# Kernel optimization log

Measured on AMD Instinct MI355X. Metric: run time of the kernel, lower is better.

The kernel has to match this reference:

```python
import jax, jax.numpy as jnp
import numpy as np

B, T = 128, 2048
E, OUT, HID = 8, 32, 64          # num_experts, kan_out_features, gru_hidden_dim
GRID_SIZE, ORDER = 5, 3          # standard efficient-kan defaults
KCOEF = GRID_SIZE + ORDER        # B-spline basis functions per input feature


def make_grid():
    # extended knot grid on [-1, 1], length GRID_SIZE + 2*ORDER + 1
    h = 2.0 / GRID_SIZE
    return jnp.arange(-ORDER, GRID_SIZE + ORDER + 1, dtype=jnp.float32) * h - 1.0


def b_splines(x, grid):
    # x: [..., in_features] -> [..., in_features, KCOEF] via Cox-de Boor recursion
    x = x[..., None]
    b = ((x >= grid[:-1]) & (x < grid[1:])).astype(x.dtype)
    for k in range(1, ORDER + 1):
        left = (x - grid[:-(k + 1)]) / (grid[k:-1] - grid[:-(k + 1)])
        right = (grid[k + 1:] - x) / (grid[k + 1:] - grid[1:-k])
        b = left * b[..., :-1] + right * b[..., 1:]
    return b


def kan_moe(x, gate_w, gate_b, base_w, spline_w, grid):
    # x: [B,T,in=1]; dense softmax-gated mixture of KANLinear experts
    gate = jax.nn.softmax(x @ gate_w + gate_b, axis=-1)                 # [B,T,E]
    base_out = jnp.einsum('bti,eoi->bteo', jax.nn.silu(x), base_w)      # [B,T,E,OUT]
    bs = b_splines(x, grid).reshape(x.shape[0], x.shape[1], -1)         # [B,T,in*KCOEF]
    spline_out = jnp.einsum('btk,eok->bteo', bs, spline_w)              # [B,T,E,OUT]
    return jnp.einsum('bte,bteo->bto', gate, base_out + spline_out)     # [B,T,OUT]


def gru(x, w_ih, w_hh, b_ih, b_hh):
    # PyTorch GRU convention: gates ordered (r, z, n); batch_first semantics
    xp = jnp.einsum('btf,gf->btg', x, w_ih) + b_ih                      # [B,T,3H]

    def step(h, xt):
        hp = h @ w_hh.T + b_hh
        xr, xz, xn = jnp.split(xt, 3, axis=-1)
        hr, hz, hn = jnp.split(hp, 3, axis=-1)
        r = jax.nn.sigmoid(xr + hr)
        z = jax.nn.sigmoid(xz + hz)
        n = jnp.tanh(xn + r * hn)
        h = (1.0 - z) * n + z * h
        return h, h

    h0 = jnp.zeros((x.shape[0], HID), x.dtype)
    _, hs = jax.lax.scan(step, h0, jnp.swapaxes(xp, 0, 1))
    return jnp.swapaxes(hs, 0, 1)                                       # [B,T,H]


def setup_inputs() -> dict:
    key = jax.random.key(0)
    ks = jax.random.split(key, 12)
    def n(k, shape, scale=0.1):
        return jax.random.normal(k, shape, jnp.float32) * scale
    return {
        'a': jax.random.normal(ks[0], (B, T, 1), jnp.float32),
        'd': jax.random.normal(ks[1], (B, T, 1), jnp.float32),
        'gate_w_a': n(ks[2], (1, E)), 'gate_b_a': jnp.zeros((E,), jnp.float32),
        'base_w_a': n(ks[3], (E, OUT, 1)), 'spline_w_a': n(ks[4], (E, OUT, KCOEF)),
        'gate_w_d': n(ks[5], (1, E)), 'gate_b_d': jnp.zeros((E,), jnp.float32),
        'base_w_d': n(ks[6], (E, OUT, 1)), 'spline_w_d': n(ks[7], (E, OUT, KCOEF)),
        'conv_w': n(ks[8], (OUT, OUT, 5)), 'conv_b': jnp.zeros((OUT,), jnp.float32),
        'w_ih': n(ks[9], (3 * HID, OUT)), 'w_hh': n(ks[10], (3 * HID, HID)),
        'b_ih': jnp.zeros((3 * HID,), jnp.float32), 'b_hh': jnp.zeros((3 * HID,), jnp.float32),
    }


def reference(a, d, gate_w_a, gate_b_a, base_w_a, spline_w_a,
              gate_w_d, gate_b_d, base_w_d, spline_w_d,
              conv_w, conv_b, w_ih, w_hh, b_ih, b_hh):
    grid = make_grid()
    fa = kan_moe(a, gate_w_a, gate_b_a, base_w_a, spline_w_a, grid)     # trend features
    fd = kan_moe(d, gate_w_d, gate_b_d, base_w_d, spline_w_d, grid)     # residual features
    # TemporalBlock: permute -> Conv1d(padding='same') -> ReLU -> permute back
    xc = jnp.swapaxes(fa, 1, 2)                                         # [B,C,T]
    yc = jax.lax.conv_general_dilated(
        xc, conv_w, (1,), 'SAME', dimension_numbers=('NCH', 'OIH', 'NCH')
    ) + conv_b[None, :, None]
    trend = jnp.swapaxes(jax.nn.relu(yc), 1, 2)                         # [B,T,OUT]
    ctx = gru(fd, w_ih, w_hh, b_ih, b_hh)                               # [B,T,HID]
    # dropout is identity in eval mode
    return jnp.concatenate([trend, ctx], axis=-1)                       # [B,T,OUT+HID]
```

## Files before the change

### kernel.cpp

```cpp
#include <hip/hip_runtime.h>
#include <cstdint>

typedef _Float16 half2_t __attribute__((ext_vector_type(2)));

#define B_   128
#define T_   2048
#define E_   8
#define OUT_ 32
#define HID_ 64
#define KC_  8
#define TILE_A 128
#define NSEG 2
#define SPLIT 1088
#define WUPC 4
#define CH_  32
#define NCHB 34

__device__ __forceinline__ float frcp(float x) { return __builtin_amdgcn_rcpf(x); }
__device__ __forceinline__ float exp2_(float x) {
#if __has_builtin(__builtin_amdgcn_exp2f)
  return __builtin_amdgcn_exp2f(x);
#else
  return exp2f(x);
#endif
}
__device__ __forceinline__ float fsig(float x) { return frcp(1.0f + __expf(-x)); }

__device__ __forceinline__ float fdot2_(half2_t a, half2_t b, float c) {
#if __has_builtin(__builtin_amdgcn_fdot2)
  return __builtin_amdgcn_fdot2(a, b, c, false);
#else
  return fmaf((float)a.x, (float)b.x, fmaf((float)a.y, (float)b.y, c));
#endif
}

__device__ __forceinline__ half2_t u2h2(unsigned u) {
  return __builtin_bit_cast(half2_t, u);
}
__device__ __forceinline__ half2_t packh2(float a, float b) {
  half2_t h; h.x = (_Float16)a; h.y = (_Float16)b; return h;
}
__device__ __forceinline__ float rlanef(float v, int i) {
  return __int_as_float(__builtin_amdgcn_readlane(__float_as_int(v), i));
}
__device__ __forceinline__ unsigned rlaneu(unsigned v, int i) {
  return (unsigned)__builtin_amdgcn_readlane((int)v, i);
}

#define NLOG2E  (-1.4426950408889634f)
#define N2LOG2E (-2.8853900817779268f)

__device__ __forceinline__ void kan_scalars(float x, const float* gwr, const float* gbr,
                                            float& silu, float* gate, float* bs) {
  silu = x * fsig(x);
  float le[E_];
  float m = -1e30f;
#pragma unroll
  for (int e = 0; e < E_; ++e) { le[e] = fmaf(x, gwr[e], gbr[e]); m = fmaxf(m, le[e]); }
  float s = 0.f;
#pragma unroll
  for (int e = 0; e < E_; ++e) { gate[e] = __expf(le[e] - m); s += gate[e]; }
  float inv = frcp(s);
#pragma unroll
  for (int e = 0; e < E_; ++e) gate[e] *= inv;
  float g[12];
#pragma unroll
  for (int i = 0; i < 12; ++i) g[i] = (float)(i - 3) * 0.4f - 1.0f;
  float bb[11];
#pragma unroll
  for (int i = 0; i < 11; ++i) bb[i] = (x >= g[i] && x < g[i + 1]) ? 1.0f : 0.0f;
#pragma unroll
  for (int k = 1; k <= 3; ++k) {
#pragma unroll
    for (int i = 0; i < 11 - k; ++i) {
      const float dl = 1.0f / (g[i + k] - g[i]);
      const float dr = 1.0f / (g[i + k + 1] - g[i + 1]);
      float left  = (x - g[i]) * dl;
      float right = (g[i + k + 1] - x) * dr;
      bb[i] = left * bb[i] + right * bb[i + 1];
    }
  }
#pragma unroll
  for (int i = 0; i < KC_; ++i) bs[i] = bb[i];
}

__global__ __launch_bounds__(256, 1) void fused4_kernel(
    const float* __restrict__ a, const float* __restrict__ d,
    const float* __restrict__ gwa, const float* __restrict__ gba,
    const float* __restrict__ bwa, const float* __restrict__ swa,
    const float* __restrict__ gwd, const float* __restrict__ gbd,
    const float* __restrict__ bwd, const float* __restrict__ swd,
    const float* __restrict__ cw, const float* __restrict__ cb,
    const float* __restrict__ wih_g, const float* __restrict__ whh_g,
    const float* __restrict__ bih_g, const float* __restrict__ bhh_g,
    float* __restrict__ out)
{
  __shared__ __align__(16) char smem_[47360];
  const int tid = threadIdx.x;

  auto xqc = (uint2 (*)[CH_][64])smem_;
  auto hbc = (unsigned short*)(smem_ + 32768);

  const int bid = (int)blockIdx.x;
  const int b = bid & (B_ - 1);
  const int seg = bid >> 7;
  const int tstart = (seg == 0) ? 0 : (SPLIT - WUPC * CH_);
  const int wup = (seg == 0) ? 0 : WUPC;
  const int w = tid >> 6;
  const int role = (w - (bid & 3)) & 3;
  const int ln = tid & 63;
  const size_t db = (size_t)b * T_;
  float* outrow = out + db * 96 + 32;
  const uint4* hq4 = (const uint4*)hbc;

  half2_t whhp[3][32];
  float bhh3[3];
  uint4 u0, u1, u2, u3, u4, u5, u6, u7;
  if (role == 0) {
#pragma unroll
    for (int g3 = 0; g3 < 3; ++g3) {
      const float sc = (g3 == 2) ? N2LOG2E : NLOG2E;
      const int g = g3 * 64 + ln;
#pragma unroll
      for (int i = 0; i < 64; i += 4) {
        const float4 v = *(const float4*)&whh_g[(size_t)g * 64 + i];
        whhp[g3][i / 2]     = packh2(v.x * sc, v.y * sc);
        whhp[g3][i / 2 + 1] = packh2(v.z * sc, v.w * sc);
      }
      bhh3[g3] = bhh_g[g] * sc;
    }
    hbc[ln] = __builtin_bit_cast(unsigned short, (_Float16)0.0f);
    asm volatile("" ::: "memory");
    u0 = hq4[0]; u1 = hq4[1]; u2 = hq4[2]; u3 = hq4[3];
    u4 = hq4[4]; u5 = hq4[5]; u6 = hq4[6]; u7 = hq4[7];
  }

  float A_[E_];
  half2_t Beh[E_][4];
  float bihr = 0.f;
  float gwrd[E_], gbrd[E_];
  const int p3 = (role >= 1) ? (role - 1) : 0;
  if (role >= 1) {
    const float sc = (p3 == 2) ? N2LOG2E : NLOG2E;
    const int g = p3 * 64 + ln;
    float wihr[32];
#pragma unroll
    for (int i = 0; i < 32; i += 4) {
      float4 v = *(const float4*)&wih_g[(size_t)g * 32 + i];
      wihr[i] = v.x * sc; wihr[i + 1] = v.y * sc;
      wihr[i + 2] = v.z * sc; wihr[i + 3] = v.w * sc;
    }
    bihr = bih_g[g] * sc;
#pragma unroll
    for (int e = 0; e < E_; ++e) { gwrd[e] = gwd[e]; gbrd[e] = gbd[e]; }
#pragma unroll
    for (int e = 0; e < E_; ++e) {
      float acc = 0.f;
#pragma unroll 4
      for (int c = 0; c < 32; c += 4) {
        const float4 bv = *(const float4*)&bwd[e * OUT_ + c];
        acc = fmaf(wihr[c], bv.x, acc);
        acc = fmaf(wihr[c + 1], bv.y, acc);
        acc = fmaf(wihr[c + 2], bv.z, acc);
        acc = fmaf(wihr[c + 3], bv.w, acc);
      }
      A_[e] = acc;
    }
#pragma unroll
    for (int e = 0; e < E_; ++e) {
      float bk[KC_];
#pragma unroll
      for (int k = 0; k < KC_; ++k) bk[k] = 0.f;
#pragma unroll 4
      for (int c = 0; c < 32; ++c) {
        const float4 s0 = *(const float4*)&swd[(e * OUT_ + c) * KC_ + 0];
        const float4 s1 = *(const float4*)&swd[(e * OUT_ + c) * KC_ + 4];
        const float wc = wihr[c];
        bk[0] = fmaf(wc, s0.x, bk[0]); bk[1] = fmaf(wc, s0.y, bk[1]);
        bk[2] = fmaf(wc, s0.z, bk[2]); bk[3] = fmaf(wc, s0.w, bk[3]);
        bk[4] = fmaf(wc, s1.x, bk[4]); bk[5] = fmaf(wc, s1.y, bk[5]);
        bk[6] = fmaf(wc, s1.z, bk[6]); bk[7] = fmaf(wc, s1.w, bk[7]);
      }
#pragma unroll
      for (int q = 0; q < 4; ++q) Beh[e][q] = packh2(bk[2 * q], bk[2 * q + 1]);
    }
  }

  float h = 0.0f;

  for (int ic = 0; ic <= NCHB; ++ic) {
    if (role >= 1 && ic < NCHB) {
      const int p = ic & 1;
      float my_silu, my_gate[E_], my_bs[KC_];
      {
        const float x = d[db + tstart + ic * CH_ + (ln & (CH_ - 1))];
        kan_scalars(x, gwrd, gbrd, my_silu, my_gate, my_bs);
      }
      unsigned my_bsp[4];
#pragma unroll
      for (int q = 0; q < 4; ++q)
        my_bsp[q] = __builtin_bit_cast(unsigned, packh2(my_bs[2 * q], my_bs[2 * q + 1]));

#pragma unroll 2
      for (int t = 0; t < CH_; ++t) {
        const float silu_t = rlanef(my_silu, t);
        const float gv0 = rlanef(my_gate[0], t), gv1 = rlanef(my_gate[1], t);
        const float gv2 = rlanef(my_gate[2], t), gv3 = rlanef(my_gate[3], t);
        const float gv4 = rlanef(my_gate[4], t), gv5 = rlanef(my_gate[5], t);
        const float gv6 = rlanef(my_gate[6], t), gv7 = rlanef(my_gate[7], t);
        const half2_t b0 = u2h2(rlaneu(my_bsp[0], t));
        const half2_t b1 = u2h2(rlaneu(my_bsp[1], t));
        const half2_t b2 = u2h2(rlaneu(my_bsp[2], t));
        const half2_t b3 = u2h2(rlaneu(my_bsp[3], t));
        float acc = bihr;
        {
          float in0 = silu_t * A_[0];
          in0 = fdot2_(b0, Beh[0][0], in0); in0 = fdot2_(b1, Beh[0][1], in0);
          in0 = fdot2_(b2, Beh[0][2], in0); in0 = fdot2_(b3, Beh[0][3], in0);
          acc = fmaf(gv0, in0, acc);
          float in1 = silu_t * A_[1];
          in1 = fdot2_(b0, Beh[1][0], in1); in1 = fdot2_(b1, Beh[1][1], in1);
          in1 = fdot2_(b2, Beh[1][2], in1); in1 = fdot2_(b3, Beh[1][3], in1);
          acc = fmaf(gv1, in1, acc);
          float in2 = silu_t * A_[2];
          in2 = fdot2_(b0, Beh[2][0], in2); in2 = fdot2_(b1, Beh[2][1], in2);
          in2 = fdot2_(b2, Beh[2][2], in2); in2 = fdot2_(b3, Beh[2][3], in2);
          acc = fmaf(gv2, in2, acc);
          float in3 = silu_t * A_[3];
          in3 = fdot2_(b0, Beh[3][0], in3); in3 = fdot2_(b1, Beh[3][1], in3);
          in3 = fdot2_(b2, Beh[3][2], in3); in3 = fdot2_(b3, Beh[3][3], in3);
          acc = fmaf(gv3, in3, acc);
          float in4 = silu_t * A_[4];
          in4 = fdot2_(b0, Beh[4][0], in4); in4 = fdot2_(b1, Beh[4][1], in4);
          in4 = fdot2_(b2, Beh[4][2], in4); in4 = fdot2_(b3, Beh[4][3], in4);
          acc = fmaf(gv4, in4, acc);
          float in5 = silu_t * A_[5];
          in5 = fdot2_(b0, Beh[5][0], in5); in5 = fdot2_(b1, Beh[5][1], in5);
          in5 = fdot2_(b2, Beh[5][2], in5); in5 = fdot2_(b3, Beh[5][3], in5);
          acc = fmaf(gv5, in5, acc);
          float in6 = silu_t * A_[6];
          in6 = fdot2_(b0, Beh[6][0], in6); in6 = fdot2_(b1, Beh[6][1], in6);
          in6 = fdot2_(b2, Beh[6][2], in6); in6 = fdot2_(b3, Beh[6][3], in6);
          acc = fmaf(gv6, in6, acc);
          float in7 = silu_t * A_[7];
          in7 = fdot2_(b0, Beh[7][0], in7); in7 = fdot2_(b1, Beh[7][1], in7);
          in7 = fdot2_(b2, Beh[7][2], in7); in7 = fdot2_(b3, Beh[7][3], in7);
          acc = fmaf(gv7, in7, acc);
        }
        ((_Float16*)&xqc[p][t][ln])[p3] = (_Float16)acc;
      }
    }

    if (role == 0 && ic >= 1) {
      const int jc = ic - 1;
      const int p = jc & 1;
      const int tb = tstart + jc * CH_;
      const bool do_store = (jc >= wup);
      const uint2 rc0 = xqc[p][0][ln];
      half2_t rz0 = u2h2(rc0.x);
      float xr = (float)rz0.x, xz = (float)rz0.y;
      float xn = (float)__builtin_bit_cast(half2_t, rc0.y).x;
      __builtin_amdgcn_s_setprio(1);
#pragma unroll 1
      for (int s = 0; s < CH_; ++s) {
        float ar0 = bhh3[0], ar1 = xr, ar2 = 0.f, ar3 = 0.f;
        float az0 = bhh3[1], az1 = xz, az2 = 0.f, az3 = 0.f;
        float an0 = bhh3[2], an1 = 0.f, an2 = 0.f, an3 = 0.f;
        {
          const half2_t q0 = u2h2(u0.x), q1 = u2h2(u0.y), q2 = u2h2(u0.z), q3 = u2h2(u0.w);
          ar0 = fdot2_(whhp[0][0], q0, ar0); ar1 = fdot2_(whhp[0][1], q1, ar1);
          ar2 = fdot2_(whhp[0][2], q2, ar2); ar3 = fdot2_(whhp[0][3], q3, ar3);
          az0 = fdot2_(whhp[1][0], q0, az0); az1 = fdot2_(whhp[1][1], q1, az1);
          az2 = fdot2_(whhp[1][2], q2, az2); az3 = fdot2_(whhp[1][3], q3, az3);
          an0 = fdot2_(whhp[2][0], q0, an0); an1 = fdot2_(whhp[2][1], q1, an1);
          an2 = fdot2_(whhp[2][2], q2, an2); an3 = fdot2_(whhp[2][3], q3, an3);
        }
        {
          const half2_t q0 = u2h2(u1.x), q1 = u2h2(u1.y), q2 = u2h2(u1.z), q3 = u2h2(u1.w);
          ar0 = fdot2_(whhp[0][4], q0, ar0); ar1 = fdot2_(whhp[0][5], q1, ar1);
          ar2 = fdot2_(whhp[0][6], q2, ar2); ar3 = fdot2_(whhp[0][7], q3, ar3);
          az0 = fdot2_(whhp[1][4], q0, az0); az1 = fdot2_(whhp[1][5], q1, az1);
          az2 = fdot2_(whhp[1][6], q2, az2); az3 = fdot2_(whhp[1][7], q3, az3);
          an0 = fdot2_(whhp[2][4], q0, an0); an1 = fdot2_(whhp[2][5], q1, an1);
          an2 = fdot2_(whhp[2][6], q2, an2); an3 = fdot2_(whhp[2][7], q3, an3);
        }
        {
          const half2_t q0 = u2h2(u2.x), q1 = u2h2(u2.y), q2 = u2h2(u2.z), q3 = u2h2(u2.w);
          ar0 = fdot2_(whhp[0][8], q0, ar0); ar1 = fdot2_(whhp[0][9], q1, ar1);
          ar2 = fdot2_(whhp[0][10], q2, ar2); ar3 = fdot2_(whhp[0][11], q3, ar3);
          az0 = fdot2_(whhp[1][8], q0, az0); az1 = fdot2_(whhp[1][9], q1, az1);
          az2 = fdot2_(whhp[1][10], q2, az2); az3 = fdot2_(whhp[1][11], q3, az3);
          an0 = fdot2_(whhp[2][8], q0, an0); an1 = fdot2_(whhp[2][9], q1, an1);
          an2 = fdot2_(whhp[2][10], q2, an2); an3 = fdot2_(whhp[2][11], q3, an3);
        }
        {
          const half2_t q0 = u2h2(u3.x), q1 = u2h2(u3.y), q2 = u2h2(u3.z), q3 = u2h2(u3.w);
          ar0 = fdot2_(whhp[0][12], q0, ar0); ar1 = fdot2_(whhp[0][13], q1, ar1);
          ar2 = fdot2_(whhp[0][14], q2, ar2); ar3 = fdot2_(whhp[0][15], q3, ar3);
          az0 = fdot2_(whhp[1][12], q0, az0); az1 = fdot2_(whhp[1][13], q1, az1);
          az2 = fdot2_(whhp[1][14], q2, az2); az3 = fdot2_(whhp[1][15], q3, az3);
          an0 = fdot2_(whhp[2][12], q0, an0); an1 = fdot2_(whhp[2][13], q1, an1);
          an2 = fdot2_(whhp[2][14], q2, an2); an3 = fdot2_(whhp[2][15], q3, an3);
        }
        {
          const half2_t q0 = u2h2(u4.x), q1 = u2h2(u4.y), q2 = u2h2(u4.z), q3 = u2h2(u4.w);
          ar0 = fdot2_(whhp[0][16], q0, ar0); ar1 = fdot2_(whhp[0][17], q1, ar1);
          ar2 = fdot2_(whhp[0][18], q2, ar2); ar3 = fdot2_(whhp[0][19], q3, ar3);
          az0 = fdot2_(whhp[1][16], q0, az0); az1 = fdot2_(whhp[1][17], q1, az1);
          az2 = fdot2_(whhp[1][18], q2, az2); az3 = fdot2_(whhp[1][19], q3, az3);
          an0 = fdot2_(whhp[2][16], q0, an0); an1 = fdot2_(whhp[2][17], q1, an1);
          an2 = fdot2_(whhp[2][18], q2, an2); an3 = fdot2_(whhp[2][19], q3, an3);
        }
        {
          const half2_t q0 = u2h2(u5.x), q1 = u2h2(u5.y), q2 = u2h2(u5.z), q3 = u2h2(u5.w);
          ar0 = fdot2_(whhp[0][20], q0, ar0); ar1 = fdot2_(whhp[0][21], q1, ar1);
          ar2 = fdot2_(whhp[0][22], q2, ar2); ar3 = fdot2_(whhp[0][23], q3, ar3);
          az0 = fdot2_(whhp[1][20], q0, az0); az1 = fdot2_(whhp[1][21], q1, az1);
          az2 = fdot2_(whhp[1][22], q2, az2); az3 = fdot2_(whhp[1][23], q3, az3);
          an0 = fdot2_(whhp[2][20], q0, an0); an1 = fdot2_(whhp[2][21], q1, an1);
          an2 = fdot2_(whhp[2][22], q2, an2); an3 = fdot2_(whhp[2][23], q3, an3);
        }
        {
          const half2_t q0 = u2h2(u6.x), q1 = u2h2(u6.y), q2 = u2h2(u6.z), q3 = u2h2(u6.w);
          ar0 = fdot2_(whhp[0][24], q0, ar0); ar1 = fdot2_(whhp[0][25], q1, ar1);
          ar2 = fdot2_(whhp[0][26], q2, ar2); ar3 = fdot2_(whhp[0][27], q3, ar3);
          az0 = fdot2_(whhp[1][24], q0, az0); az1 = fdot2_(whhp[1][25], q1, az1);
          az2 = fdot2_(whhp[1][26], q2, az2); az3 = fdot2_(whhp[1][27], q3, az3);
          an0 = fdot2_(whhp[2][24], q0, an0); an1 = fdot2_(whhp[2][25], q1, an1);
          an2 = fdot2_(whhp[2][26], q2, an2); an3 = fdot2_(whhp[2][27], q3, an3);
        }
        {
          const half2_t q0 = u2h2(u7.x), q1 = u2h2(u7.y), q2 = u2h2(u7.z), q3 = u2h2(u7.w);
          ar0 = fdot2_(whhp[0][28], q0, ar0); ar1 = fdot2_(whhp[0][29], q1, ar1);
          ar2 = fdot2_(whhp[0][30], q2, ar2); ar3 = fdot2_(whhp[0][31], q3, ar3);
          az0 = fdot2_(whhp[1][28], q0, az0); az1 = fdot2_(whhp[1][29], q1, az1);
          az2 = fdot2_(whhp[1][30], q2, az2); az3 = fdot2_(whhp[1][31], q3, az3);
          an0 = fdot2_(whhp[2][28], q0, an0); an1 = fdot2_(whhp[2][29], q1, an1);
          an2 = fdot2_(whhp[2][30], q2, an2); an3 = fdot2_(whhp[2][31], q3, an3);
        }
        const float hr = (ar0 + ar1) + (ar2 + ar3);
        const float hz = (az0 + az1) + (az2 + az3);
        const float hn = (an0 + an1) + (an2 + an3);
        const float r = frcp(1.0f + exp2_(hr));
        const float z = frcp(1.0f + exp2_(hz));
        const float tn = frcp(1.0f + exp2_(fmaf(r, hn, xn)));
        const float n = fmaf(2.0f, tn, -1.0f);
        h = n + z * (h - n);
        hbc[ln] = __builtin_bit_cast(unsigned short, (_Float16)h);
        asm volatile("" ::: "memory");
        const int sn = (s + 1) & (CH_ - 1);
        const uint2 rcn = xqc[p][sn][ln];
        u0 = hq4[0]; u1 = hq4[1]; u2 = hq4[2]; u3 = hq4[3];
        u4 = hq4[4]; u5 = hq4[5]; u6 = hq4[6]; u7 = hq4[7];
        asm volatile("" ::: "memory");
        if (do_store) outrow[(size_t)(tb + s) * 96 + ln] = h;
        const half2_t rzh = u2h2(rcn.x);
        xr = (float)rzh.x; xz = (float)rzh.y;
        xn = (float)__builtin_bit_cast(half2_t, rcn.y).x;
      }
      __builtin_amdgcn_s_setprio(0);
    }
    __syncthreads();
  }

  {
    auto fa  = (float (*)[136])smem_;
    auto cwl = (float (*)[161])(smem_ + 17408);
    auto swl = (float (*)[OUT_][KC_])(smem_ + 38016);
    auto bwl = (float (*)[OUT_])(smem_ + 46208);
    float* gwl = (float*)(smem_ + 47232);
    float* gbl = (float*)(smem_ + 47264);

    for (int i = tid; i < OUT_ * OUT_ * 5; i += 256) cwl[i / 160][i % 160] = cw[i];
    for (int i = tid; i < E_ * OUT_ * KC_; i += 256) ((float*)swl)[i] = swa[i];
    for (int i = tid; i < E_ * OUT_; i += 256) ((float*)bwl)[i] = bwa[i];
    if (tid < E_) { gwl[tid] = gwa[tid]; gbl[tid] = gba[tid]; }
    __syncthreads();

#pragma unroll 1
    for (int it = 0; it < 8; ++it) {
      const int t0 = (seg * 8 + it) * TILE_A;
      if (tid < TILE_A + 4) {
        const int i = tid;
        const int t = t0 + i - 2;
        const bool inr = (t >= 0) && (t < T_);
        const float x = inr ? a[db + t] : 0.0f;
        float gwr[E_], gbr[E_];
#pragma unroll
        for (int e = 0; e < E_; ++e) { gwr[e] = gwl[e]; gbr[e] = gbl[e]; }
        float silu, gate[E_], bs[KC_];
        kan_scalars(x, gwr, gbr, silu, gate, bs);
#pragma unroll 4
        for (int cc = 0; cc < OUT_; ++cc) {
          float accb = 0.f, accs = 0.f;
#pragma unroll
          for (int e = 0; e < E_; ++e) {
            accb = fmaf(gate[e], bwl[e][cc], accb);
            const float4 s0 = *(const float4*)&swl[e][cc][0];
            const float4 s1 = *(const float4*)&swl[e][cc][4];
            float dot = bs[0]*s0.x + bs[1]*s0.y + bs[2]*s0.z + bs[3]*s0.w
                      + bs[4]*s1.x + bs[5]*s1.y + bs[6]*s1.z + bs[7]*s1.w;
            accs = fmaf(gate[e], dot, accs);
          }
          fa[cc][i] = inr ? fmaf(silu, accb, accs) : 0.0f;
        }
      }
      __syncthreads();
      {
        const int o = tid & 31;
        const int grp = tid >> 5;
        const float bias = cb[o];
        float acc[16];
#pragma unroll
        for (int q = 0; q < 16; ++q) acc[q] = bias;
        for (int c = 0; c < OUT_; ++c) {
          float col[20];
#pragma unroll
          for (int q = 0; q < 5; ++q)
            *(float4*)&col[q * 4] = *(const float4*)&fa[c][grp * 16 + q * 4];
#pragma unroll
          for (int jj = 0; jj < 5; ++jj) {
            const float wv = cwl[o][c * 5 + jj];
#pragma unroll
            for (int q = 0; q < 16; ++q) acc[q] = fmaf(col[q + jj], wv, acc[q]);
          }
        }
#pragma unroll
        for (int q = 0; q < 16; ++q) {
          const int t = t0 + grp * 16 + q;
          out[(db + t) * 96 + o] = fmaxf(acc[q], 0.0f);
        }
      }
      __syncthreads();
    }
  }
}

extern "C" void kernel_launch(void* const* d_in, const int* in_sizes, int n_in,
                              void* d_out, int out_size, void* d_ws, size_t ws_size,
                              hipStream_t stream) {
  (void)in_sizes; (void)n_in; (void)out_size; (void)d_ws; (void)ws_size;
  const float* a        = (const float*)d_in[0];
  const float* d        = (const float*)d_in[1];
  const float* gate_w_a = (const float*)d_in[2];
  const float* gate_b_a = (const float*)d_in[3];
  const float* base_w_a = (const float*)d_in[4];
  const float* spln_w_a = (const float*)d_in[5];
  const float* gate_w_d = (const float*)d_in[6];
  const float* gate_b_d = (const float*)d_in[7];
  const float* base_w_d = (const float*)d_in[8];
  const float* spln_w_d = (const float*)d_in[9];
  const float* conv_w   = (const float*)d_in[10];
  const float* conv_b   = (const float*)d_in[11];
  const float* w_ih     = (const float*)d_in[12];
  const float* w_hh     = (const float*)d_in[13];
  const float* b_ih     = (const float*)d_in[14];
  const float* b_hh     = (const float*)d_in[15];
  float* out = (float*)d_out;

  fused4_kernel<<<NSEG * B_, 256, 0, stream>>>(
      a, d, gate_w_a, gate_b_a, base_w_a, spln_w_a,
      gate_w_d, gate_b_d, base_w_d, spln_w_d,
      conv_w, conv_b, w_ih, w_hh, b_ih, b_hh, out);
}
```

Baseline: 564.2 us.

## Merge both time segments into one 512-thread block per batch row

Each batch row now gets a single 512-thread block instead of two 256-thread blocks, one per time segment. Inside the block, waves 0 and 7 run the two GRU recurrences and the other six waves produce input projections for their own segment. The shared-memory staging of projections is split into an r/z array and a separate n array. The trend KAN-plus-conv tail now walks all 16 tiles, with each thread computing 8 timesteps instead of 16. This halves the grid to 128 blocks, which may leave half the CUs idle and serialises more of the trend tail, and it drops the rotation of wave roles across SIMDs.

```diff
diff --git a/kernel.cpp b/kernel.cpp
--- a/kernel.cpp
+++ b/kernel.cpp
@@ -10,7 +10,6 @@
 #define HID_ 64
 #define KC_  8
 #define TILE_A 128
-#define NSEG 2
 #define SPLIT 1088
 #define WUPC 4
 #define CH_  32
@@ -84,7 +83,7 @@
   for (int i = 0; i < KC_; ++i) bs[i] = bb[i];
 }
 
-__global__ __launch_bounds__(256, 1) void fused4_kernel(
+__global__ __launch_bounds__(512, 1) void fused7_kernel(
     const float* __restrict__ a, const float* __restrict__ d,
     const float* __restrict__ gwa, const float* __restrict__ gba,
     const float* __restrict__ bwa, const float* __restrict__ swa,
@@ -95,28 +94,30 @@
     const float* __restrict__ bih_g, const float* __restrict__ bhh_g,
     float* __restrict__ out)
 {
-  __shared__ __align__(16) char smem_[47360];
+  __shared__ __align__(16) char smem_[49664];
   const int tid = threadIdx.x;
 
-  auto xqc = (uint2 (*)[CH_][64])smem_;
-  auto hbc = (unsigned short*)(smem_ + 32768);
-
-  const int bid = (int)blockIdx.x;
-  const int b = bid & (B_ - 1);
-  const int seg = bid >> 7;
-  const int tstart = (seg == 0) ? 0 : (SPLIT - WUPC * CH_);
-  const int wup = (seg == 0) ? 0 : WUPC;
+  auto xqrz = (unsigned (*)[2][CH_][64])smem_;
+  auto xqn  = (_Float16 (*)[2][CH_][64])(smem_ + 32768);
+  auto hbc  = (unsigned short (*)[64])(smem_ + 49152);
+
+  const int b = (int)blockIdx.x;
   const int w = tid >> 6;
-  const int role = (w - (bid & 3)) & 3;
   const int ln = tid & 63;
+  const int myseg = (w >= 4) ? 1 : 0;
+  const bool is_cons = (w == 0) || (w == 7);
+  const bool is_prod = !is_cons;
+  const int p3 = is_prod ? (myseg ? (w - 4) : (w - 1)) : 0;
+  const int tstart = myseg ? (SPLIT - WUPC * CH_) : 0;
+  const int wup = myseg ? WUPC : 0;
   const size_t db = (size_t)b * T_;
   float* outrow = out + db * 96 + 32;
-  const uint4* hq4 = (const uint4*)hbc;
+  const uint4* hq4 = (const uint4*)&hbc[myseg][0];
 
   half2_t whhp[3][32];
   float bhh3[3];
   uint4 u0, u1, u2, u3, u4, u5, u6, u7;
-  if (role == 0) {
+  if (is_cons) {
 #pragma unroll
     for (int g3 = 0; g3 < 3; ++g3) {
       const float sc = (g3 == 2) ? N2LOG2E : NLOG2E;
@@ -129,7 +130,7 @@
       }
       bhh3[g3] = bhh_g[g] * sc;
     }
-    hbc[ln] = __builtin_bit_cast(unsigned short, (_Float16)0.0f);
+    hbc[myseg][ln] = __builtin_bit_cast(unsigned short, (_Float16)0.0f);
     asm volatile("" ::: "memory");
     u0 = hq4[0]; u1 = hq4[1]; u2 = hq4[2]; u3 = hq4[3];
     u4 = hq4[4]; u5 = hq4[5]; u6 = hq4[6]; u7 = hq4[7];
@@ -139,8 +140,7 @@
   half2_t Beh[E_][4];
   float bihr = 0.f;
   float gwrd[E_], gbrd[E_];
-  const int p3 = (role >= 1) ? (role - 1) : 0;
-  if (role >= 1) {
+  if (is_prod) {
     const float sc = (p3 == 2) ? N2LOG2E : NLOG2E;
     const int g = p3 * 64 + ln;
     float wihr[32];
@@ -189,7 +189,7 @@
   float h = 0.0f;
 
   for (int ic = 0; ic <= NCHB; ++ic) {
-    if (role >= 1 && ic < NCHB) {
+    if (is_prod && ic < NCHB) {
       const int p = ic & 1;
       float my_silu, my_gate[E_], my_bs[KC_];
       {
@@ -247,19 +247,19 @@
           in7 = fdot2_(b2, Beh[7][2], in7); in7 = fdot2_(b3, Beh[7][3], in7);
           acc = fmaf(gv7, in7, acc);
         }
-        ((_Float16*)&xqc[p][t][ln])[p3] = (_Float16)acc;
-      }
-    }
-
-    if (role == 0 && ic >= 1) {
+        if (p3 < 2) ((_Float16*)&xqrz[myseg][p][t][ln])[p3] = (_Float16)acc;
+        else        xqn[myseg][p][t][ln] = (_Float16)acc;
+      }
+    }
+
+    if (is_cons && ic >= 1) {
       const int jc = ic - 1;
       const int p = jc & 1;
       const int tb = tstart + jc * CH_;
       const bool do_store = (jc >= wup);
-      const uint2 rc0 = xqc[p][0][ln];
-      half2_t rz0 = u2h2(rc0.x);
+      half2_t rz0 = u2h2(xqrz[myseg][p][0][ln]);
       float xr = (float)rz0.x, xz = (float)rz0.y;
-      float xn = (float)__builtin_bit_cast(half2_t, rc0.y).x;
+      float xn = (float)xqn[myseg][p][0][ln];
       __builtin_amdgcn_s_setprio(1);
 #pragma unroll 1
       for (int s = 0; s < CH_; ++s) {
@@ -346,17 +346,17 @@
         const float tn = frcp(1.0f + exp2_(fmaf(r, hn, xn)));
         const float n = fmaf(2.0f, tn, -1.0f);
         h = n + z * (h - n);
-        hbc[ln] = __builtin_bit_cast(unsigned short, (_Float16)h);
+        hbc[myseg][ln] = __builtin_bit_cast(unsigned short, (_Float16)h);
         asm volatile("" ::: "memory");
         const int sn = (s + 1) & (CH_ - 1);
-        const uint2 rcn = xqc[p][sn][ln];
+        const unsigned rzn = xqrz[myseg][p][sn][ln];
+        const _Float16 xnn = xqn[myseg][p][sn][ln];
         u0 = hq4[0]; u1 = hq4[1]; u2 = hq4[2]; u3 = hq4[3];
         u4 = hq4[4]; u5 = hq4[5]; u6 = hq4[6]; u7 = hq4[7];
         asm volatile("" ::: "memory");
         if (do_store) outrow[(size_t)(tb + s) * 96 + ln] = h;
-        const half2_t rzh = u2h2(rcn.x);
-        xr = (float)rzh.x; xz = (float)rzh.y;
-        xn = (float)__builtin_bit_cast(half2_t, rcn.y).x;
+        const half2_t rzh = u2h2(rzn);
+        xr = (float)rzh.x; xz = (float)rzh.y; xn = (float)xnn;
       }
       __builtin_amdgcn_s_setprio(0);
     }
@@ -371,15 +371,15 @@
     float* gwl = (float*)(smem_ + 47232);
     float* gbl = (float*)(smem_ + 47264);
 
-    for (int i = tid; i < OUT_ * OUT_ * 5; i += 256) cwl[i / 160][i % 160] = cw[i];
-    for (int i = tid; i < E_ * OUT_ * KC_; i += 256) ((float*)swl)[i] = swa[i];
-    for (int i = tid; i < E_ * OUT_; i += 256) ((float*)bwl)[i] = bwa[i];
+    for (int i = tid; i < OUT_ * OUT_ * 5; i += 512) cwl[i / 160][i % 160] = cw[i];
+    for (int i = tid; i < E_ * OUT_ * KC_; i += 512) ((float*)swl)[i] = swa[i];
+    for (int i = tid; i < E_ * OUT_; i += 512) ((float*)bwl)[i] = bwa[i];
     if (tid < E_) { gwl[tid] = gwa[tid]; gbl[tid] = gba[tid]; }
     __syncthreads();
 
 #pragma unroll 1
-    for (int it = 0; it < 8; ++it) {
-      const int t0 = (seg * 8 + it) * TILE_A;
+    for (int it = 0; it < 16; ++it) {
+      const int t0 = it * TILE_A;
       if (tid < TILE_A + 4) {
         const int i = tid;
         const int t = t0 + i - 2;
@@ -410,24 +410,24 @@
         const int o = tid & 31;
         const int grp = tid >> 5;
         const float bias = cb[o];
-        float acc[16];
-#pragma unroll
-        for (int q = 0; q < 16; ++q) acc[q] = bias;
+        float acc[8];
+#pragma unroll
+        for (int q = 0; q < 8; ++q) acc[q] = bias;
         for (int c = 0; c < OUT_; ++c) {
-          float col[20];
-#pragma unroll
-          for (int q = 0; q < 5; ++q)
-            *(float4*)&col[q * 4] = *(const float4*)&fa[c][grp * 16 + q * 4];
+          float col[12];
+#pragma unroll
+          for (int q = 0; q < 3; ++q)
+            *(float4*)&col[q * 4] = *(const float4*)&fa[c][grp * 8 + q * 4];
 #pragma unroll
           for (int jj = 0; jj < 5; ++jj) {
             const float wv = cwl[o][c * 5 + jj];
 #pragma unroll
-            for (int q = 0; q < 16; ++q) acc[q] = fmaf(col[q + jj], wv, acc[q]);
+            for (int q = 0; q < 8; ++q) acc[q] = fmaf(col[q + jj], wv, acc[q]);
           }
         }
 #pragma unroll
-        for (int q = 0; q < 16; ++q) {
-          const int t = t0 + grp * 16 + q;
+        for (int q = 0; q < 8; ++q) {
+          const int t = t0 + grp * 8 + q;
           out[(db + t) * 96 + o] = fmaxf(acc[q], 0.0f);
         }
       }
@@ -458,7 +458,7 @@
   const float* b_hh     = (const float*)d_in[15];
   float* out = (float*)d_out;
 
-  fused4_kernel<<<NSEG * B_, 256, 0, stream>>>(
+  fused7_kernel<<<B_, 512, 0, stream>>>(
       a, d, gate_w_a, gate_b_a, base_w_a, spln_w_a,
       gate_w_d, gate_b_d, base_w_d, spln_w_d,
       conv_w, conv_b, w_ih, w_hh, b_ih, b_hh, out);
```

Measured after the change: 715.5 us. 1.27x slower.

## Split fused kernel into precompute, projection-fill and segmented GRU kernels

Applied to the files above, without the earlier changes.

Moves the GRU input projection out of the recurrent kernel into a separate massively parallel kernel that writes fp16 projections to workspace, with a tiny kernel folding the KAN weights into the GRU input weights once. The recurrence then runs in four time segments with warm-up steps, each a single-wave block, so the serial step count per block shrinks. The conv/trend branch is computed by extra blocks of the fill kernel. This trades extra HBM traffic through the workspace and more launches for a shorter serial critical path; it falls back to the old fused kernel if the workspace is too small.

```diff
diff --git a/kernel.cpp b/kernel.cpp
--- a/kernel.cpp
+++ b/kernel.cpp
@@ -10,7 +10,19 @@
 #define HID_ 64
 #define KC_  8
 #define TILE_A 128
-#define NSEG 2
+
+#define NSEG4 4
+#define SEG0OUT 608
+#define SEGOUT 480
+#define WUPS 128
+#define NSTEPS 608
+#define XQ_BYTES ((size_t)B_ * T_ * 3 * 64 * 2)
+#define FOLD_AF   0
+#define FOLD_BU   6144
+#define FOLD_BIH  30720
+#define FOLD_BYTES 31488
+#define WS_NEED (XQ_BYTES + FOLD_BYTES)
+
 #define SPLIT 1088
 #define WUPC 4
 #define CH_  32
@@ -82,6 +94,351 @@
   }
 #pragma unroll
   for (int i = 0; i < KC_; ++i) bs[i] = bb[i];
+}
+
+__global__ __launch_bounds__(256) void fold_kernel(
+    const float* __restrict__ bwd, const float* __restrict__ swd,
+    const float* __restrict__ wih_g, const float* __restrict__ bih_g,
+    char* __restrict__ fold)
+{
+  const int g = threadIdx.x;
+  if (g >= 192) return;
+  float* Af   = (float*)(fold + FOLD_AF);
+  unsigned* Bu = (unsigned*)(fold + FOLD_BU);
+  float* bihf = (float*)(fold + FOLD_BIH);
+  const float sc = (g >= 128) ? N2LOG2E : NLOG2E;
+  float wihr[32];
+#pragma unroll 4
+  for (int i = 0; i < 32; ++i) wihr[i] = wih_g[(size_t)g * 32 + i] * sc;
+  bihf[g] = bih_g[g] * sc;
+#pragma unroll
+  for (int e = 0; e < E_; ++e) {
+    float acc = 0.f;
+#pragma unroll 4
+    for (int c = 0; c < 32; ++c) acc = fmaf(wihr[c], bwd[e * OUT_ + c], acc);
+    Af[g * 8 + e] = acc;
+    float bk[KC_];
+#pragma unroll
+    for (int k = 0; k < KC_; ++k) bk[k] = 0.f;
+#pragma unroll 4
+    for (int c = 0; c < 32; ++c) {
+      const float wc = wihr[c];
+#pragma unroll
+      for (int k = 0; k < KC_; ++k) bk[k] = fmaf(wc, swd[(e * OUT_ + c) * KC_ + k], bk[k]);
+    }
+#pragma unroll
+    for (int q = 0; q < 4; ++q)
+      Bu[g * 32 + e * 4 + q] = __builtin_bit_cast(unsigned, packh2(bk[2 * q], bk[2 * q + 1]));
+  }
+}
+
+__global__ __launch_bounds__(256) void xqfill_kernel(
+    const float* __restrict__ a, const float* __restrict__ d,
+    const float* __restrict__ gwa, const float* __restrict__ gba,
+    const float* __restrict__ bwa, const float* __restrict__ swa,
+    const float* __restrict__ gwd, const float* __restrict__ gbd,
+    const float* __restrict__ cw, const float* __restrict__ cb,
+    char* __restrict__ ws, float* __restrict__ out)
+{
+  const int tid = threadIdx.x;
+  const int bid = (int)blockIdx.x;
+  if (bid < 4096) {
+    const int w = tid >> 6;
+    if (w == 3) return;
+    const int ln = tid & 63;
+    const int b = bid >> 5;
+    const int tile = bid & 31;
+    _Float16* XQ = (_Float16*)ws;
+    const float* Af   = (const float*)(ws + XQ_BYTES + FOLD_AF);
+    const unsigned* Bu = (const unsigned*)(ws + XQ_BYTES + FOLD_BU);
+    const float* bihf = (const float*)(ws + XQ_BYTES + FOLD_BIH);
+    const int g = w * 64 + ln;
+    float A_[E_];
+    half2_t Beh[E_][4];
+#pragma unroll
+    for (int e = 0; e < E_; ++e) {
+      A_[e] = Af[g * 8 + e];
+#pragma unroll
+      for (int q = 0; q < 4; ++q) Beh[e][q] = u2h2(Bu[g * 32 + e * 4 + q]);
+    }
+    const float bihr = bihf[g];
+    float gwrd[E_], gbrd[E_];
+#pragma unroll
+    for (int e = 0; e < E_; ++e) { gwrd[e] = gwd[e]; gbrd[e] = gbd[e]; }
+    float my_silu, my_gate[E_], my_bs[KC_];
+    {
+      const float x = d[(size_t)b * T_ + tile * 64 + ln];
+      kan_scalars(x, gwrd, gbrd, my_silu, my_gate, my_bs);
+    }
+    unsigned my_bsp[4];
+#pragma unroll
+    for (int q = 0; q < 4; ++q)
+      my_bsp[q] = __builtin_bit_cast(unsigned, packh2(my_bs[2 * q], my_bs[2 * q + 1]));
+#pragma unroll 2
+    for (int it = 0; it < 64; ++it) {
+      const float silu_t = rlanef(my_silu, it);
+      const float gv0 = rlanef(my_gate[0], it), gv1 = rlanef(my_gate[1], it);
+      const float gv2 = rlanef(my_gate[2], it), gv3 = rlanef(my_gate[3], it);
+      const float gv4 = rlanef(my_gate[4], it), gv5 = rlanef(my_gate[5], it);
+      const float gv6 = rlanef(my_gate[6], it), gv7 = rlanef(my_gate[7], it);
+      const half2_t b0 = u2h2(rlaneu(my_bsp[0], it));
+      const half2_t b1 = u2h2(rlaneu(my_bsp[1], it));
+      const half2_t b2 = u2h2(rlaneu(my_bsp[2], it));
+      const half2_t b3 = u2h2(rlaneu(my_bsp[3], it));
+      float acc = bihr;
+      {
+        float in0 = silu_t * A_[0];
+        in0 = fdot2_(b0, Beh[0][0], in0); in0 = fdot2_(b1, Beh[0][1], in0);
+        in0 = fdot2_(b2, Beh[0][2], in0); in0 = fdot2_(b3, Beh[0][3], in0);
+        acc = fmaf(gv0, in0, acc);
+        float in1 = silu_t * A_[1];
+        in1 = fdot2_(b0, Beh[1][0], in1); in1 = fdot2_(b1, Beh[1][1], in1);
+        in1 = fdot2_(b2, Beh[1][2], in1); in1 = fdot2_(b3, Beh[1][3], in1);
+        acc = fmaf(gv1, in1, acc);
+        float in2 = silu_t * A_[2];
+        in2 = fdot2_(b0, Beh[2][0], in2); in2 = fdot2_(b1, Beh[2][1], in2);
+        in2 = fdot2_(b2, Beh[2][2], in2); in2 = fdot2_(b3, Beh[2][3], in2);
+        acc = fmaf(gv2, in2, acc);
+        float in3 = silu_t * A_[3];
+        in3 = fdot2_(b0, Beh[3][0], in3); in3 = fdot2_(b1, Beh[3][1], in3);
+        in3 = fdot2_(b2, Beh[3][2], in3); in3 = fdot2_(b3, Beh[3][3], in3);
+        acc = fmaf(gv3, in3, acc);
+        float in4 = silu_t * A_[4];
+        in4 = fdot2_(b0, Beh[4][0], in4); in4 = fdot2_(b1, Beh[4][1], in4);
+        in4 = fdot2_(b2, Beh[4][2], in4); in4 = fdot2_(b3, Beh[4][3], in4);
+        acc = fmaf(gv4, in4, acc);
+        float in5 = silu_t * A_[5];
+        in5 = fdot2_(b0, Beh[5][0], in5); in5 = fdot2_(b1, Beh[5][1], in5);
+        in5 = fdot2_(b2, Beh[5][2], in5); in5 = fdot2_(b3, Beh[5][3], in5);
+        acc = fmaf(gv5, in5, acc);
+        float in6 = silu_t * A_[6];
+        in6 = fdot2_(b0, Beh[6][0], in6); in6 = fdot2_(b1, Beh[6][1], in6);
+        in6 = fdot2_(b2, Beh[6][2], in6); in6 = fdot2_(b3, Beh[6][3], in6);
+        acc = fmaf(gv6, in6, acc);
+        float in7 = silu_t * A_[7];
+        in7 = fdot2_(b0, Beh[7][0], in7); in7 = fdot2_(b1, Beh[7][1], in7);
+        in7 = fdot2_(b2, Beh[7][2], in7); in7 = fdot2_(b3, Beh[7][3], in7);
+        acc = fmaf(gv7, in7, acc);
+      }
+      const int t = tile * 64 + it;
+      XQ[(((size_t)b * T_ + t) * 3 + w) * 64 + ln] = (_Float16)acc;
+    }
+  } else {
+    __shared__ __align__(16) char smem_[47360];
+    auto fa  = (float (*)[136])smem_;
+    auto cwl = (float (*)[161])(smem_ + 17408);
+    auto swl = (float (*)[OUT_][KC_])(smem_ + 38016);
+    auto bwl = (float (*)[OUT_])(smem_ + 46208);
+    float* gwl = (float*)(smem_ + 47232);
+    float* gbl = (float*)(smem_ + 47264);
+    for (int i = tid; i < OUT_ * OUT_ * 5; i += 256) cwl[i / 160][i % 160] = cw[i];
+    for (int i = tid; i < E_ * OUT_ * KC_; i += 256) ((float*)swl)[i] = swa[i];
+    for (int i = tid; i < E_ * OUT_; i += 256) ((float*)bwl)[i] = bwa[i];
+    if (tid < E_) { gwl[tid] = gwa[tid]; gbl[tid] = gba[tid]; }
+    __syncthreads();
+    const int cid = bid - 4096;
+#pragma unroll 1
+    for (int it = 0; it < 16; ++it) {
+      const int gt = cid + it * 128;
+      const int bb = gt >> 4;
+      const int t0 = (gt & 15) * TILE_A;
+      if (tid < TILE_A + 4) {
+        const int i = tid;
+        const int t = t0 + i - 2;
+        const bool inr = (t >= 0) && (t < T_);
+        const float x = inr ? a[(size_t)bb * T_ + t] : 0.0f;
+        float gwr[E_], gbr[E_];
+#pragma unroll
+        for (int e = 0; e < E_; ++e) { gwr[e] = gwl[e]; gbr[e] = gbl[e]; }
+        float silu, gate[E_], bs[KC_];
+        kan_scalars(x, gwr, gbr, silu, gate, bs);
+#pragma unroll 4
+        for (int cc = 0; cc < OUT_; ++cc) {
+          float accb = 0.f, accs = 0.f;
+#pragma unroll
+          for (int e = 0; e < E_; ++e) {
+            accb = fmaf(gate[e], bwl[e][cc], accb);
+            const float4 s0 = *(const float4*)&swl[e][cc][0];
+            const float4 s1 = *(const float4*)&swl[e][cc][4];
+            float dot = bs[0]*s0.x + bs[1]*s0.y + bs[2]*s0.z + bs[3]*s0.w
+                      + bs[4]*s1.x + bs[5]*s1.y + bs[6]*s1.z + bs[7]*s1.w;
+            accs = fmaf(gate[e], dot, accs);
+          }
+          fa[cc][i] = inr ? fmaf(silu, accb, accs) : 0.0f;
+        }
+      }
+      __syncthreads();
+      {
+        const int o = tid & 31;
+        const int grp = tid >> 5;
+        const float bias = cb[o];
+        float acc[16];
+#pragma unroll
+        for (int q = 0; q < 16; ++q) acc[q] = bias;
+        for (int c = 0; c < OUT_; ++c) {
+          float col[20];
+#pragma unroll
+          for (int q = 0; q < 5; ++q)
+            *(float4*)&col[q * 4] = *(const float4*)&fa[c][grp * 16 + q * 4];
+#pragma unroll
+          for (int jj = 0; jj < 5; ++jj) {
+            const float wv = cwl[o][c * 5 + jj];
+#pragma unroll
+            for (int q = 0; q < 16; ++q) acc[q] = fmaf(col[q + jj], wv, acc[q]);
+          }
+        }
+#pragma unroll
+        for (int q = 0; q < 16; ++q) {
+          const int t = t0 + grp * 16 + q;
+          out[((size_t)bb * T_ + t) * 96 + o] = fmaxf(acc[q], 0.0f);
+        }
+      }
+      __syncthreads();
+    }
+  }
+}
+
+__global__ __launch_bounds__(64, 1) void gru_consume_kernel(
+    const char* __restrict__ ws, const float* __restrict__ whh_g,
+    const float* __restrict__ bhh_g, float* __restrict__ out)
+{
+  __shared__ __align__(16) unsigned short hbc[64];
+  const int bid = (int)blockIdx.x;
+  const int seg = bid >> 7;
+  const int b = bid & (B_ - 1);
+  const int ln = threadIdx.x & 63;
+  const int tstart = (seg == 0) ? 0 : (SEGOUT * seg);
+  const int wupsteps = (seg == 0) ? 0 : WUPS;
+  const size_t db = (size_t)b * T_;
+  const _Float16* XQ = (const _Float16*)ws;
+  float* outrow = out + db * 96 + 32;
+  const uint4* hq4 = (const uint4*)hbc;
+
+  half2_t whhp[3][32];
+  float bhh3[3];
+#pragma unroll
+  for (int g3 = 0; g3 < 3; ++g3) {
+    const float sc = (g3 == 2) ? N2LOG2E : NLOG2E;
+    const int g = g3 * 64 + ln;
+#pragma unroll
+    for (int i = 0; i < 64; i += 4) {
+      const float4 v = *(const float4*)&whh_g[(size_t)g * 64 + i];
+      whhp[g3][i / 2]     = packh2(v.x * sc, v.y * sc);
+      whhp[g3][i / 2 + 1] = packh2(v.z * sc, v.w * sc);
+    }
+    bhh3[g3] = bhh_g[g] * sc;
+  }
+  hbc[ln] = __builtin_bit_cast(unsigned short, (_Float16)0.0f);
+  asm volatile("" ::: "memory");
+  uint4 u0 = hq4[0], u1 = hq4[1], u2 = hq4[2], u3 = hq4[3];
+  uint4 u4 = hq4[4], u5 = hq4[5], u6 = hq4[6], u7 = hq4[7];
+
+  float h = 0.0f;
+  const _Float16* xq0 = XQ + ((db + tstart) * 3) * 64 + ln;
+  float xr = (float)xq0[0];
+  float xz = (float)xq0[64];
+  float xn = (float)xq0[128];
+
+  __builtin_amdgcn_s_setprio(1);
+#pragma unroll 1
+  for (int s = 0; s < NSTEPS; ++s) {
+    float ar0 = bhh3[0], ar1 = xr, ar2 = 0.f, ar3 = 0.f;
+    float az0 = bhh3[1], az1 = xz, az2 = 0.f, az3 = 0.f;
+    float an0 = bhh3[2], an1 = 0.f, an2 = 0.f, an3 = 0.f;
+    {
+      const half2_t q0 = u2h2(u0.x), q1 = u2h2(u0.y), q2 = u2h2(u0.z), q3 = u2h2(u0.w);
+      ar0 = fdot2_(whhp[0][0], q0, ar0); ar1 = fdot2_(whhp[0][1], q1, ar1);
+      ar2 = fdot2_(whhp[0][2], q2, ar2); ar3 = fdot2_(whhp[0][3], q3, ar3);
+      az0 = fdot2_(whhp[1][0], q0, az0); az1 = fdot2_(whhp[1][1], q1, az1);
+      az2 = fdot2_(whhp[1][2], q2, az2); az3 = fdot2_(whhp[1][3], q3, az3);
+      an0 = fdot2_(whhp[2][0], q0, an0); an1 = fdot2_(whhp[2][1], q1, an1);
+      an2 = fdot2_(whhp[2][2], q2, an2); an3 = fdot2_(whhp[2][3], q3, an3);
+    }
+    {
+      const half2_t q0 = u2h2(u1.x), q1 = u2h2(u1.y), q2 = u2h2(u1.z), q3 = u2h2(u1.w);
+      ar0 = fdot2_(whhp[0][4], q0, ar0); ar1 = fdot2_(whhp[0][5], q1, ar1);
+      ar2 = fdot2_(whhp[0][6], q2, ar2); ar3 = fdot2_(whhp[0][7], q3, ar3);
+      az0 = fdot2_(whhp[1][4], q0, az0); az1 = fdot2_(whhp[1][5], q1, az1);
+      az2 = fdot2_(whhp[1][6], q2, az2); az3 = fdot2_(whhp[1][7], q3, az3);
+      an0 = fdot2_(whhp[2][4], q0, an0); an1 = fdot2_(whhp[2][5], q1, an1);
+      an2 = fdot2_(whhp[2][6], q2, an2); an3 = fdot2_(whhp[2][7], q3, an3);
+    }
+    {
+      const half2_t q0 = u2h2(u2.x), q1 = u2h2(u2.y), q2 = u2h2(u2.z), q3 = u2h2(u2.w);
+      ar0 = fdot2_(whhp[0][8], q0, ar0); ar1 = fdot2_(whhp[0][9], q1, ar1);
+      ar2 = fdot2_(whhp[0][10], q2, ar2); ar3 = fdot2_(whhp[0][11], q3, ar3);
+      az0 = fdot2_(whhp[1][8], q0, az0); az1 = fdot2_(whhp[1][9], q1, az1);
+      az2 = fdot2_(whhp[1][10], q2, az2); az3 = fdot2_(whhp[1][11], q3, az3);
+      an0 = fdot2_(whhp[2][8], q0, an0); an1 = fdot2_(whhp[2][9], q1, an1);
+      an2 = fdot2_(whhp[2][10], q2, an2); an3 = fdot2_(whhp[2][11], q3, an3);
+    }
+    {
+      const half2_t q0 = u2h2(u3.x), q1 = u2h2(u3.y), q2 = u2h2(u3.z), q3 = u2h2(u3.w);
+      ar0 = fdot2_(whhp[0][12], q0, ar0); ar1 = fdot2_(whhp[0][13], q1, ar1);
+      ar2 = fdot2_(whhp[0][14], q2, ar2); ar3 = fdot2_(whhp[0][15], q3, ar3);
+      az0 = fdot2_(whhp[1][12], q0, az0); az1 = fdot2_(whhp[1][13], q1, az1);
+      az2 = fdot2_(whhp[1][14], q2, az2); az3 = fdot2_(whhp[1][15], q3, az3);
+      an0 = fdot2_(whhp[2][12], q0, an0); an1 = fdot2_(whhp[2][13], q1, an1);
+      an2 = fdot2_(whhp[2][14], q2, an2); an3 = fdot2_(whhp[2][15], q3, an3);
+    }
+    {
+      const half2_t q0 = u2h2(u4.x), q1 = u2h2(u4.y), q2 = u2h2(u4.z), q3 = u2h2(u4.w);
+      ar0 = fdot2_(whhp[0][16], q0, ar0); ar1 = fdot2_(whhp[0][17], q1, ar1);
+      ar2 = fdot2_(whhp[0][18], q2, ar2); ar3 = fdot2_(whhp[0][19], q3, ar3);
+      az0 = fdot2_(whhp[1][16], q0, az0); az1 = fdot2_(whhp[1][17], q1, az1);
+      az2 = fdot2_(whhp[1][18], q2, az2); az3 = fdot2_(whhp[1][19], q3, az3);
+      an0 = fdot2_(whhp[2][16], q0, an0); an1 = fdot2_(whhp[2][17], q1, an1);
+      an2 = fdot2_(whhp[2][18], q2, an2); an3 = fdot2_(whhp[2][19], q3, an3);
+    }
+    {
+      const half2_t q0 = u2h2(u5.x), q1 = u2h2(u5.y), q2 = u2h2(u5.z), q3 = u2h2(u5.w);
+      ar0 = fdot2_(whhp[0][20], q0, ar0); ar1 = fdot2_(whhp[0][21], q1, ar1);
+      ar2 = fdot2_(whhp[0][22], q2, ar2); ar3 = fdot2_(whhp[0][23], q3, ar3);
+      az0 = fdot2_(whhp[1][20], q0, az0); az1 = fdot2_(whhp[1][21], q1, az1);
+      az2 = fdot2_(whhp[1][22], q2, az2); az3 = fdot2_(whhp[1][23], q3, az3);
+      an0 = fdot2_(whhp[2][20], q0, an0); an1 = fdot2_(whhp[2][21], q1, an1);
+      an2 = fdot2_(whhp[2][22], q2, an2); an3 = fdot2_(whhp[2][23], q3, an3);
+    }
+    {
+      const half2_t q0 = u2h2(u6.x), q1 = u2h2(u6.y), q2 = u2h2(u6.z), q3 = u2h2(u6.w);
+      ar0 = fdot2_(whhp[0][24], q0, ar0); ar1 = fdot2_(whhp[0][25], q1, ar1);
+      ar2 = fdot2_(whhp[0][26], q2, ar2); ar3 = fdot2_(whhp[0][27], q3, ar3);
+      az0 = fdot2_(whhp[1][24], q0, az0); az1 = fdot2_(whhp[1][25], q1, az1);
+      az2 = fdot2_(whhp[1][26], q2, az2); az3 = fdot2_(whhp[1][27], q3, az3);
+      an0 = fdot2_(whhp[2][24], q0, an0); an1 = fdot2_(whhp[2][25], q1, an1);
+      an2 = fdot2_(whhp[2][26], q2, an2); an3 = fdot2_(whhp[2][27], q3, an3);
+    }
+    {
+      const half2_t q0 = u2h2(u7.x), q1 = u2h2(u7.y), q2 = u2h2(u7.z), q3 = u2h2(u7.w);
+      ar0 = fdot2_(whhp[0][28], q0, ar0); ar1 = fdot2_(whhp[0][29], q1, ar1);
+      ar2 = fdot2_(whhp[0][30], q2, ar2); ar3 = fdot2_(whhp[0][31], q3, ar3);
+      az0 = fdot2_(whhp[1][28], q0, az0); az1 = fdot2_(whhp[1][29], q1, az1);
+      az2 = fdot2_(whhp[1][30], q2, az2); az3 = fdot2_(whhp[1][31], q3, az3);
+      an0 = fdot2_(whhp[2][28], q0, an0); an1 = fdot2_(whhp[2][29], q1, an1);
+      an2 = fdot2_(whhp[2][30], q2, an2); an3 = fdot2_(whhp[2][31], q3, an3);
+    }
+    const float hr = (ar0 + ar1) + (ar2 + ar3);
+    const float hz = (az0 + az1) + (az2 + az3);
+    const float hn = (an0 + an1) + (an2 + an3);
+    const float r = frcp(1.0f + exp2_(hr));
+    const float z = frcp(1.0f + exp2_(hz));
+    const float tn = frcp(1.0f + exp2_(fmaf(r, hn, xn)));
+    const float n = fmaf(2.0f, tn, -1.0f);
+    h = n + z * (h - n);
+    hbc[ln] = __builtin_bit_cast(unsigned short, (_Float16)h);
+    asm volatile("" ::: "memory");
+    const int t = tstart + s;
+    const _Float16* xqn_ = XQ + ((db + t + 1) * 3) * 64 + ln;
+    const _Float16 xr_n = (s < NSTEPS - 1) ? xqn_[0]   : (_Float16)0.f;
+    const _Float16 xz_n = (s < NSTEPS - 1) ? xqn_[64]  : (_Float16)0.f;
+    const _Float16 xn_n = (s < NSTEPS - 1) ? xqn_[128] : (_Float16)0.f;
+    u0 = hq4[0]; u1 = hq4[1]; u2 = hq4[2]; u3 = hq4[3];
+    u4 = hq4[4]; u5 = hq4[5]; u6 = hq4[6]; u7 = hq4[7];
+    asm volatile("" ::: "memory");
+    if (s >= wupsteps) outrow[(size_t)t * 96 + ln] = h;
+    xr = (float)xr_n; xz = (float)xz_n; xn = (float)xn_n;
+  }
+  __builtin_amdgcn_s_setprio(0);
 }
 
 __global__ __launch_bounds__(256, 1) void fused4_kernel(
@@ -97,10 +454,8 @@
 {
   __shared__ __align__(16) char smem_[47360];
   const int tid = threadIdx.x;
-
   auto xqc = (uint2 (*)[CH_][64])smem_;
   auto hbc = (unsigned short*)(smem_ + 32768);
-
   const int bid = (int)blockIdx.x;
   const int b = bid & (B_ - 1);
   const int seg = bid >> 7;
@@ -112,7 +467,6 @@
   const size_t db = (size_t)b * T_;
   float* outrow = out + db * 96 + 32;
   const uint4* hq4 = (const uint4*)hbc;
-
   half2_t whhp[3][32];
   float bhh3[3];
   uint4 u0, u1, u2, u3, u4, u5, u6, u7;
@@ -134,7 +488,6 @@
     u0 = hq4[0]; u1 = hq4[1]; u2 = hq4[2]; u3 = hq4[3];
     u4 = hq4[4]; u5 = hq4[5]; u6 = hq4[6]; u7 = hq4[7];
   }
-
   float A_[E_];
   half2_t Beh[E_][4];
   float bihr = 0.f;
@@ -185,9 +538,7 @@
       for (int q = 0; q < 4; ++q) Beh[e][q] = packh2(bk[2 * q], bk[2 * q + 1]);
     }
   }
-
   float h = 0.0f;
-
   for (int ic = 0; ic <= NCHB; ++ic) {
     if (role >= 1 && ic < NCHB) {
       const int p = ic & 1;
@@ -200,7 +551,6 @@
 #pragma unroll
       for (int q = 0; q < 4; ++q)
         my_bsp[q] = __builtin_bit_cast(unsigned, packh2(my_bs[2 * q], my_bs[2 * q + 1]));
-
 #pragma unroll 2
       for (int t = 0; t < CH_; ++t) {
         const float silu_t = rlanef(my_silu, t);
@@ -250,7 +600,6 @@
         ((_Float16*)&xqc[p][t][ln])[p3] = (_Float16)acc;
       }
     }
-
     if (role == 0 && ic >= 1) {
       const int jc = ic - 1;
       const int p = jc & 1;
@@ -362,7 +711,6 @@
     }
     __syncthreads();
   }
-
   {
     auto fa  = (float (*)[136])smem_;
     auto cwl = (float (*)[161])(smem_ + 17408);
@@ -370,13 +718,11 @@
     auto bwl = (float (*)[OUT_])(smem_ + 46208);
     float* gwl = (float*)(smem_ + 47232);
     float* gbl = (float*)(smem_ + 47264);
-
     for (int i = tid; i < OUT_ * OUT_ * 5; i += 256) cwl[i / 160][i % 160] = cw[i];
     for (int i = tid; i < E_ * OUT_ * KC_; i += 256) ((float*)swl)[i] = swa[i];
     for (int i = tid; i < E_ * OUT_; i += 256) ((float*)bwl)[i] = bwa[i];
     if (tid < E_) { gwl[tid] = gwa[tid]; gbl[tid] = gba[tid]; }
     __syncthreads();
-
 #pragma unroll 1
     for (int it = 0; it < 8; ++it) {
       const int t0 = (seg * 8 + it) * TILE_A;
@@ -439,7 +785,7 @@
 extern "C" void kernel_launch(void* const* d_in, const int* in_sizes, int n_in,
                               void* d_out, int out_size, void* d_ws, size_t ws_size,
                               hipStream_t stream) {
-  (void)in_sizes; (void)n_in; (void)out_size; (void)d_ws; (void)ws_size;
+  (void)in_sizes; (void)n_in; (void)out_size;
   const float* a        = (const float*)d_in[0];
   const float* d        = (const float*)d_in[1];
   const float* gate_w_a = (const float*)d_in[2];
@@ -458,8 +804,16 @@
   const float* b_hh     = (const float*)d_in[15];
   float* out = (float*)d_out;
 
-  fused4_kernel<<<NSEG * B_, 256, 0, stream>>>(
-      a, d, gate_w_a, gate_b_a, base_w_a, spln_w_a,
-      gate_w_d, gate_b_d, base_w_d, spln_w_d,
-      conv_w, conv_b, w_ih, w_hh, b_ih, b_hh, out);
-}
+  if (ws_size >= WS_NEED && d_ws != nullptr) {
+    char* ws = (char*)d_ws;
+    fold_kernel<<<1, 256, 0, stream>>>(base_w_d, spln_w_d, w_ih, b_ih, ws + XQ_BYTES);
+    xqfill_kernel<<<4224, 256, 0, stream>>>(a, d, gate_w_a, gate_b_a, base_w_a, spln_w_a,
+                                            gate_w_d, gate_b_d, conv_w, conv_b, ws, out);
+    gru_consume_kernel<<<512, 64, 0, stream>>>(ws, w_hh, b_hh, out);
+  } else {
+    fused4_kernel<<<2 * B_, 256, 0, stream>>>(
+        a, d, gate_w_a, gate_b_a, base_w_a, spln_w_a,
+        gate_w_d, gate_b_d, base_w_d, spln_w_d,
+        conv_w, conv_b, w_ih, w_hh, b_ih, b_hh, out);
+  }
+}
```

Result: slower. 950.4 us (+68.4%).
